# Kernel optimization log

Hardware: AMD Instinct MI355X
Metric: run time of the kernel (lower is better)

## Reference

```python
import jax, jax.numpy as jnp
import numpy as np

MIN_NORM = 1e-15
BALL_EPS = 4e-3  # fp32 boundary eps used by HGCN PoincareBall.proj
C = 1.0
RATIO = 0.75


def _norm(x):
    return jnp.clip(jnp.sqrt(jnp.sum(x * x, axis=-1, keepdims=True)), MIN_NORM)


def artanh(x):
    return jnp.arctanh(jnp.clip(x, -1.0 + 1e-7, 1.0 - 1e-7))


def proj(x, c):
    n = _norm(x)
    maxnorm = (1.0 - BALL_EPS) / jnp.sqrt(c)
    return jnp.where(n > maxnorm, x / n * maxnorm, x)


def expmap0(u, c):
    sc = jnp.sqrt(c)
    un = _norm(u)
    return jnp.tanh(sc * un) * u / (sc * un)


def logmap0(p, c):
    sc = jnp.sqrt(c)
    pn = _norm(p)
    return artanh(sc * pn) * p / (sc * pn)


def mobius_matvec(m, x, c):
    sc = jnp.sqrt(c)
    xn = _norm(x)
    mx = x @ m.T  # [N, out]
    mxn = _norm(mx)
    res = jnp.tanh(mxn / xn * artanh(sc * xn)) * mx / (mxn * sc)
    zero = jnp.all(mx == 0, axis=-1, keepdims=True)
    return jnp.where(zero, jnp.zeros_like(res), res)


def mobius_add(x, y, c):
    x2 = jnp.sum(x * x, axis=-1, keepdims=True)
    y2 = jnp.sum(y * y, axis=-1, keepdims=True)
    xy = jnp.sum(x * y, axis=-1, keepdims=True)
    num = (1 + 2 * c * xy + c * y2) * x + (1 - c * x2) * y
    den = 1 + 2 * c * xy + c * c * x2 * y2
    return num / jnp.maximum(den, MIN_NORM)


def hyp_linear(x, W, b, c):
    res = proj(mobius_matvec(W, x, c), c)
    hb = proj(expmap0(b[None, :], c), c)  # proj_tan0 is identity in Poincare ball
    return proj(mobius_add(res, hb, c), c)


def setup_inputs() -> dict:
    key = jax.random.key(0)
    k = jax.random.split(key, 6)
    N, E, D_IN, D_OUT = 50000, 800000, 128, 64
    x = 0.01 * jax.random.normal(k[0], (N, D_IN), jnp.float32)  # points near origin of ball
    W = jax.random.normal(k[1], (D_OUT, D_IN), jnp.float32) * np.sqrt(2.0 / (D_IN + D_OUT))
    b = 0.01 * jax.random.normal(k[2], (D_OUT,), jnp.float32)
    beta_W = jax.random.normal(k[3], (1, 2 * D_OUT), jnp.float32) * np.sqrt(2.0 / (2 * D_OUT + 1))
    beta_b = 0.01 * jax.random.normal(k[4], (1,), jnp.float32)
    edge_index = jax.random.randint(k[5], (2, E), 0, N, dtype=jnp.int64)
    return {"x": x, "W": W, "b": b, "beta_W": beta_W, "beta_b": beta_b, "edge_index": edge_index}


def reference(x, W, b, beta_W, beta_b, edge_index):
    N = x.shape[0]
    src, dst = edge_index[0], edge_index[1]  # PyG: x_j = x[src], aggregated at dst
    agg = lambda v: jax.ops.segment_sum(v[src], dst, num_segments=N)

    updated_x = hyp_linear(x, W, b, C)
    updated_tanx = logmap0(updated_x, C)

    # NodeInformationScore: (I - D^{-1/2} A D^{-1/2}) x, self loops removed (weight 0)
    w = jnp.where(src == dst, 0.0, 1.0).astype(x.dtype)
    deg = jax.ops.segment_sum(w, src, num_segments=N)
    dinv = jnp.where(deg > 0, deg ** -0.5, 0.0)
    norm_e = dinv[src] * w * dinv[dst]  # [E]
    neigh = jax.ops.segment_sum(norm_e[:, None] * updated_tanx[src], dst, num_segments=N)
    info = updated_tanx - neigh
    score = jnp.sum(jnp.abs(info), axis=1)  # [N]

    k = int(N * RATIO)
    T = jax.lax.top_k(score, k)[0][-1]  # min of top-k values
    sel = (score > T).astype(x.dtype)[:, None]  # [N, 1] hard gate

    sum_neigh = agg(updated_tanx)
    sum_sel = agg(sel * updated_tanx)
    concat = jnp.concatenate([sum_sel, sum_neigh], axis=-1)  # [N, 2*out]
    hyp_sums = proj(expmap0(concat, C), C)

    beta_out = hyp_linear(hyp_sums, beta_W, beta_b, C)  # [N, 1]
    w_sel = jax.nn.sigmoid(logmap0(beta_out, C))  # [N, 1]

    A_x = jax.nn.relu(agg(w_sel * sel * updated_tanx))
    out = proj(expmap0(updated_tanx + A_x, C), C)
    return out
```

## Files before the change

kernel.cpp:

```cpp
#include <hip/hip_runtime.h>
#include <math.h>
#include <limits.h>


__device__ __forceinline__ float wredsum(float v) {
#pragma unroll
    for (int off = 32; off > 0; off >>= 1) v += __shfl_xor(v, off, 64);
    return v;
}

__device__ __forceinline__ float rdlane_f(float v, int i) {
    return __uint_as_float(__builtin_amdgcn_readlane(__float_as_uint(v), i));
}

__device__ __forceinline__ int bitonic64(int val, int lane) {
#pragma unroll
    for (int k = 2; k <= 64; k <<= 1) {
#pragma unroll
        for (int j = k >> 1; j > 0; j >>= 1) {
            int other = __shfl_xor(val, j, 64);
            bool asc = ((lane & k) == 0);
            bool lower = ((lane & j) == 0);
            val = (asc == lower) ? min(val, other) : max(val, other);
        }
    }
    return val;
}

__device__ __forceinline__ float artanh_pos(float z) {
    z = fminf(z, 1.0f - 1e-7f);
    return 0.5f * (log1pf(z) - log1pf(-z));
}

__device__ __forceinline__ unsigned short f2bf(float f) {
    unsigned u = __float_as_uint(f);
    unsigned r = 0x7FFFu + ((u >> 16) & 1u);
    return (unsigned short)((u + r) >> 16);
}
__device__ __forceinline__ float bf2f(unsigned short h) {
    return __uint_as_float(((unsigned)h) << 16);
}

#define MAXNORM 0.996f
#define MINNORM 1e-15f
#define SLOT    64
#define GRP_CAP 5120


__global__ void k_transW(const float* __restrict__ W, float* __restrict__ WT) {
    int idx = blockIdx.x * 256 + threadIdx.x;
    if (idx >= 64 * 128) return;
    int o = idx >> 7, k = idx & 127;
    WT[k * 64 + o] = W[idx];
}


__global__ __launch_bounds__(256) void k_linear(
    const float* __restrict__ x, const float* __restrict__ WTg,
    const float* __restrict__ b, float* __restrict__ utx,
    unsigned short* __restrict__ utx16, int N)
{
    __shared__ float wt[8192];
    __shared__ float xq4[4][64];
    __shared__ float hb_s[64];
    int tid = threadIdx.x;
    int wave = tid >> 6, lane = tid & 63;
    int wave_u = __builtin_amdgcn_readfirstlane(wave);
    int r_hi = lane >> 3, o_hi = lane & 7;

    {
        const float4* src = (const float4*)WTg;
        float4* dst = (float4*)wt;
        for (int i = tid; i < 2048; i += 256) dst[i] = src[i];
    }
    if (wave == 0) {
        float bv = b[lane];
        float bn = fmaxf(sqrtf(wredsum(bv * bv)), MINNORM);
        float h = tanhf(bn) / bn * bv;
        float hn = fmaxf(sqrtf(wredsum(h * h)), MINNORM);
        if (hn > MAXNORM) h *= MAXNORM / hn;
        hb_s[lane] = h;
    }
    __syncthreads();

    int rbase = blockIdx.x * 64;
    const float4* xr4[8];
#pragma unroll
    for (int j = 0; j < 8; ++j)
        xr4[j] = (const float4*)(x + (size_t)min(rbase + r_hi * 8 + j, N - 1) * 128);

    float acc[64];
#pragma unroll
    for (int e = 0; e < 64; ++e) acc[e] = 0.f;
    float xsq8[8];
#pragma unroll
    for (int j = 0; j < 8; ++j) xsq8[j] = 0.f;

    int kb = wave_u * 32;
    for (int q = 0; q < 8; ++q) {
        int c = wave_u * 8 + q;
        float4 xq[8];
#pragma unroll
        for (int j = 0; j < 8; ++j)
            xq[j] = xr4[j][c];
        float wreg[4][8];
#pragma unroll
        for (int i = 0; i < 4; ++i) {
            float4 lo = *(const float4*)(wt + (kb + q * 4 + i) * 64 + o_hi * 8);
            float4 hi = *(const float4*)(wt + (kb + q * 4 + i) * 64 + o_hi * 8 + 4);
            wreg[i][0] = lo.x; wreg[i][1] = lo.y; wreg[i][2] = lo.z; wreg[i][3] = lo.w;
            wreg[i][4] = hi.x; wreg[i][5] = hi.y; wreg[i][6] = hi.z; wreg[i][7] = hi.w;
        }
#pragma unroll
        for (int j = 0; j < 8; ++j) {
#pragma unroll
            for (int oj = 0; oj < 8; ++oj) {
                acc[j * 8 + oj] += xq[j].x * wreg[0][oj] + xq[j].y * wreg[1][oj]
                                 + xq[j].z * wreg[2][oj] + xq[j].w * wreg[3][oj];
            }
            xsq8[j] += xq[j].x * xq[j].x + xq[j].y * xq[j].y
                     + xq[j].z * xq[j].z + xq[j].w * xq[j].w;
        }
    }

    if (o_hi == 0) {
#pragma unroll
        for (int j = 0; j < 8; ++j) xq4[wave_u][r_hi * 8 + j] = xsq8[j];
    }
    __syncthreads();

    float* redp = wt;
#pragma unroll
    for (int c = 0; c < 4; ++c) {
        if (wave_u != 0) {
#pragma unroll
            for (int r = 0; r < 16; ++r) redp[(wave_u - 1) * 1024 + r * 64 + lane] = acc[c * 16 + r];
        }
        __syncthreads();
        if (wave_u == 0) {
#pragma unroll
            for (int r = 0; r < 16; ++r)
                acc[c * 16 + r] += redp[0 * 1024 + r * 64 + lane]
                                 + redp[1 * 1024 + r * 64 + lane]
                                 + redp[2 * 1024 + r * 64 + lane];
        }
        __syncthreads();
    }

    float* eT = wt + 3072;
    if (wave_u == 0) {
#pragma unroll
        for (int j = 0; j < 8; ++j) {
            float4 v0 = { acc[j * 8 + 0], acc[j * 8 + 1], acc[j * 8 + 2], acc[j * 8 + 3] };
            float4 v1 = { acc[j * 8 + 4], acc[j * 8 + 5], acc[j * 8 + 6], acc[j * 8 + 7] };
            *(float4*)(eT + (r_hi * 8 + j) * 68 + o_hi * 8) = v0;
            *(float4*)(eT + (r_hi * 8 + j) * 68 + o_hi * 8 + 4) = v1;
        }
    }
    __syncthreads();
    if (wave_u != 0) return;

    float a2[64];
#pragma unroll
    for (int c4 = 0; c4 < 16; ++c4) {
        float4 v = *(const float4*)(eT + lane * 68 + c4 * 4);
        a2[c4 * 4 + 0] = v.x; a2[c4 * 4 + 1] = v.y;
        a2[c4 * 4 + 2] = v.z; a2[c4 * 4 + 3] = v.w;
    }
    float xsq = xq4[0][lane];
    xsq += xq4[1][lane] + xq4[2][lane] + xq4[3][lane];

    int row = blockIdx.x * 64 + lane;
    bool valid = row < N;

    float mx2 = 0.f;
#pragma unroll
    for (int o = 0; o < 64; ++o) mx2 += a2[o] * a2[o];

    float xn  = fmaxf(sqrtf(xsq), MINNORM);
    float mxn = fmaxf(sqrtf(mx2), MINNORM);
    float fac = tanhf(mxn / xn * artanh_pos(xn)) / mxn;
    float rn  = fac * mxn;
    if (rn > MAXNORM) { fac *= MAXNORM / rn; rn = MAXNORM; }
    float x2 = rn * rn;

    float hv_ = hb_s[lane];
    float hb2 = wredsum(hv_ * hv_);

    float xy = 0.f;
#pragma unroll
    for (int o = 0; o < 64; ++o) xy += (fac * a2[o]) * hb_s[o];

    float den = fmaxf(1.f + 2.f * xy + x2 * hb2, MINNORM);
    float ca  = (1.f + 2.f * xy + hb2) / den;
    float cb  = (1.f - x2) / den;

    float pn2 = 0.f;
#pragma unroll
    for (int o = 0; o < 64; ++o) {
        float p = ca * (fac * a2[o]) + cb * hb_s[o];
        a2[o] = p;
        pn2 += p * p;
    }
    float pn  = fmaxf(sqrtf(pn2), MINNORM);
    float psc = (pn > MAXNORM) ? (MAXNORM / pn) : 1.0f;
    float qn  = fmaxf(pn * psc, MINNORM);
    float lfac = artanh_pos(qn) / qn * psc;

    if (valid) {
        float* orow = utx + (size_t)row * 64;
        unsigned short* orow16 = utx16 + (size_t)row * 64;
#pragma unroll
        for (int o = 0; o < 64; o += 4) {
            float4 ov = { a2[o] * lfac, a2[o + 1] * lfac,
                          a2[o + 2] * lfac, a2[o + 3] * lfac };
            *(float4*)(orow + o) = ov;
            ushort4 hv = { f2bf(ov.x), f2bf(ov.y), f2bf(ov.z), f2bf(ov.w) };
            *(ushort4*)(orow16 + o) = hv;
        }
    }
}


__global__ __launch_bounds__(256) void k_partA(
    const int* __restrict__ ei, int E,
    int* cursD, int* cursS, unsigned* __restrict__ recD,
    unsigned char* __restrict__ recS)
{
    __shared__ int hD[256], hS[256], bD[256], bS[256];
    int tid = threadIdx.x;
    hD[tid] = 0; hS[tid] = 0;
    __syncthreads();
    int base = blockIdx.x * 4096;
    int sv[16], dv[16];
#pragma unroll
    for (int i = 0; i < 16; ++i) {
        int e = base + tid + i * 256;
        if (e < E) {
            sv[i] = ei[e]; dv[i] = ei[E + e];
            atomicAdd(&hD[dv[i] >> 8], 1);
            if (sv[i] != dv[i]) atomicAdd(&hS[sv[i] >> 8], 1);
        } else sv[i] = -1;
    }
    __syncthreads();
    if (hD[tid]) bD[tid] = atomicAdd(&cursD[tid], hD[tid]);
    if (hS[tid]) bS[tid] = atomicAdd(&cursS[tid], hS[tid]);
    __syncthreads();
    hD[tid] = 0; hS[tid] = 0;
    __syncthreads();
#pragma unroll
    for (int i = 0; i < 16; ++i) {
        if (sv[i] < 0) continue;
        int gD = dv[i] >> 8;
        int p = bD[gD] + atomicAdd(&hD[gD], 1);
        if (p < GRP_CAP)
            recD[(size_t)gD * GRP_CAP + p] = (unsigned)sv[i] | ((unsigned)(dv[i] & 255) << 16);
        if (sv[i] != dv[i]) {
            int gS = sv[i] >> 8;
            int q = bS[gS] + atomicAdd(&hS[gS], 1);
            if (q < GRP_CAP)
                recS[(size_t)gS * GRP_CAP + q] = (unsigned char)(sv[i] & 255);
        }
    }
}

__global__ __launch_bounds__(256) void k_Bdeg(
    const int* __restrict__ cursS, const unsigned char* __restrict__ recS,
    float* __restrict__ dinv, int N)
{
    __shared__ unsigned h[256];
    int g = blockIdx.x, tid = threadIdx.x;
    h[tid] = 0;
    __syncthreads();
    int m = min(cursS[g], GRP_CAP);
    const unsigned char* r = recS + (size_t)g * GRP_CAP;
    for (int i = tid; i < m; i += 256) atomicAdd(&h[r[i]], 1u);
    __syncthreads();
    int n = g * 256 + tid;
    if (n < N) {
        unsigned dg = h[tid];
        dinv[n] = dg > 0 ? 1.0f / sqrtf((float)dg) : 0.0f;
    }
}

__global__ __launch_bounds__(256) void k_Bscat(
    const int* __restrict__ cursD, const unsigned* __restrict__ recD,
    int* __restrict__ cnt, int* __restrict__ slots, int N)
{
    __shared__ int lcnt[256];
    __shared__ int lslot[256 * SLOT];
    int g = blockIdx.x, tid = threadIdx.x;
    lcnt[tid] = 0;
    __syncthreads();
    int m = min(cursD[g], GRP_CAP);
    const unsigned* r = recD + (size_t)g * GRP_CAP;
    for (int i = tid; i < m; i += 256) {
        unsigned v = r[i];
        int dlo = v >> 16, s = (int)(v & 0xFFFFu);
        int p = atomicAdd(&lcnt[dlo], 1);
        if (p < SLOT) lslot[dlo * SLOT + p] = s;
    }
    __syncthreads();
    int nbase = g * 256;
    if (nbase + tid < N) cnt[nbase + tid] = lcnt[tid];
    int wave = tid >> 6, lane = tid & 63;
    for (int j = 0; j < 64; ++j) {
        int node = wave * 64 + j;
        if (nbase + node >= N) break;
        int d = min(lcnt[node], SLOT);
        if (lane < d)
            slots[(size_t)(nbase + node) * SLOT + lane] = lslot[node * SLOT + lane];
    }
}


__global__ __launch_bounds__(256) void k_pass1(
    const float* __restrict__ utx, const int* __restrict__ cnt,
    const int* __restrict__ slots, const float* __restrict__ dinv,
    float* __restrict__ score, float* __restrict__ sumn, int N)
{
    int wid = (blockIdx.x * 256 + threadIdx.x) >> 6;
    int lane = threadIdx.x & 63;
    if (wid >= N) return;
    int d = min(cnt[wid], SLOT);
    int val = (lane < d) ? slots[(size_t)wid * SLOT + lane] : INT_MAX;
    val = bitonic64(val, lane);
    int sval = (lane < d) ? val : wid;
    float dn = dinv[wid];
    float wv = (lane < d && sval != wid) ? dn * dinv[sval] : 0.f;
    float wn = (lane < d) ? 1.0f : 0.0f;

    float accn = 0.f, accs = 0.f;
    for (int i0 = 0; i0 < d; i0 += 8) {
#pragma unroll
        for (int j = 0; j < 8; ++j) {
            int i = i0 + j;
            int   s = __builtin_amdgcn_readlane(sval, i);
            float w = rdlane_f(wv, i);
            float n = rdlane_f(wn, i);
            float v = utx[(size_t)s * 64 + lane];
            accn += w * v;
            accs += n * v;
        }
    }
    float info = utx[(size_t)wid * 64 + lane] - accn;
    float sc = wredsum(fabsf(info));
    sumn[(size_t)wid * 64 + lane] = accs;
    if (lane == 0) score[wid] = sc;
}


__global__ __launch_bounds__(256) void k_hist8(
    const float* __restrict__ score, unsigned* __restrict__ hist,
    const unsigned* __restrict__ scal, int N, int pass)
{
    __shared__ unsigned lh[256];
    int tid = threadIdx.x;
    lh[tid] = 0;
    __syncthreads();
    int n = blockIdx.x * 256 + tid;
    if (n < N) {
        unsigned bits = __float_as_uint(score[n]);
        bool active = (pass == 0) || (((bits ^ scal[0]) >> (32 - 8 * pass)) == 0u);
        if (active) atomicAdd(&lh[(bits >> (24 - 8 * pass)) & 0xFFu], 1u);
    }
    __syncthreads();
    unsigned c = lh[tid];
    if (c) atomicAdd(&hist[tid], c);
}

__global__ __launch_bounds__(256) void k_pick8(
    const unsigned* __restrict__ hist, unsigned* scal, int K, int pass)
{
    __shared__ unsigned h[256];
    int t = threadIdx.x;
    h[t] = hist[t];
    __syncthreads();
    if (t == 0) {
        unsigned R = (pass == 0) ? (unsigned)K : scal[1];
        unsigned acc = 0;
        int B = 0;
        for (int bin = 255; bin >= 0; --bin) {
            if (acc + h[bin] >= R) { B = bin; break; }
            acc += h[bin];
        }
        unsigned prefix = (pass == 0) ? 0u : scal[0];
        scal[0] = prefix | ((unsigned)B << (24 - 8 * pass));
        scal[1] = R - acc;
        if (pass == 3) scal[2] = scal[0];
    }
}


__global__ __launch_bounds__(256) void k_sums_corr(
    const unsigned short* __restrict__ utx16, const int* __restrict__ cnt,
    const int* __restrict__ slots, const float* __restrict__ score,
    const unsigned* __restrict__ scal,
    const float* __restrict__ sumn, float* __restrict__ sums, int N)
{
    int wid = (blockIdx.x * 256 + threadIdx.x) >> 6;
    int lane = threadIdx.x & 63;
    if (wid >= N) return;
    float T = __uint_as_float(scal[2]);
    int d = min(cnt[wid], SLOT);
    int val = (lane < d) ? slots[(size_t)wid * SLOT + lane] : INT_MAX;
    val = bitonic64(val, lane);
    int sval = (lane < d) ? val : wid;
    float wc = (lane < d) ? ((score[sval] > T) ? 0.0f : 1.0f) : 0.0f;

    float corr = 0.f;
    for (int i0 = 0; i0 < d; i0 += 8) {
#pragma unroll
        for (int j = 0; j < 8; ++j) {
            int i = i0 + j;
            float w = rdlane_f(wc, i);
            int   s = __builtin_amdgcn_readlane(sval, i);
            if (w != 0.f)
                corr += bf2f(utx16[(size_t)s * 64 + lane]);
        }
    }
    size_t o = (size_t)wid * 64 + lane;
    sums[o] = sumn[o] - corr;
}


__global__ __launch_bounds__(256) void k_beta(
    const float* __restrict__ sumn, const float* __restrict__ sums,
    const float* __restrict__ beta_W, const float* __restrict__ beta_b,
    const float* __restrict__ score, const unsigned* __restrict__ scal,
    float* __restrict__ wsel, int N)
{
    int n = blockIdx.x * 256 + threadIdx.x;
    if (n >= N) return;
    const float4* su4 = (const float4*)(sums + (size_t)n * 64);
    const float4* sn4 = (const float4*)(sumn + (size_t)n * 64);
    float s_uu = 0.f, s_ub = 0.f;
#pragma unroll
    for (int k4 = 0; k4 < 16; ++k4) {
        float4 u0 = su4[k4];
        float4 u1 = sn4[k4];
        float4 b0 = *(const float4*)(beta_W + k4 * 4);
        float4 b1 = *(const float4*)(beta_W + 64 + k4 * 4);
        s_uu += u0.x * u0.x + u0.y * u0.y + u0.z * u0.z + u0.w * u0.w
              + u1.x * u1.x + u1.y * u1.y + u1.z * u1.z + u1.w * u1.w;
        s_ub += u0.x * b0.x + u0.y * b0.y + u0.z * b0.z + u0.w * b0.w
              + u1.x * b1.x + u1.y * b1.y + u1.z * b1.z + u1.w * b1.w;
    }
    float un = fmaxf(sqrtf(s_uu), MINNORM);
    float f  = tanhf(un) / un;
    float hn = fmaxf(f * un, MINNORM);
    float psc1 = (hn > MAXNORM) ? (MAXNORM / hn) : 1.0f;
    float xn = fmaxf(hn * psc1, MINNORM);
    float mx = f * psc1 * s_ub;
    float mxn = fmaxf(fabsf(mx), MINNORM);
    float res = tanhf(mxn / xn * artanh_pos(xn)) * mx / mxn;
    float rn = fmaxf(fabsf(res), MINNORM);
    if (rn > MAXNORM) res = res / rn * MAXNORM;
    float bb = beta_b[0];
    float bn = fmaxf(fabsf(bb), MINNORM);
    float hb = tanhf(bn) / bn * bb;
    float hbn = fmaxf(fabsf(hb), MINNORM);
    if (hbn > MAXNORM) hb = hb / hbn * MAXNORM;
    float x2 = res * res, y2 = hb * hb, xy = res * hb;
    float num = (1.f + 2.f * xy + y2) * res + (1.f - x2) * hb;
    float den = 1.f + 2.f * xy + x2 * y2;
    float p = num / fmaxf(den, MINNORM);
    float pn = fmaxf(fabsf(p), MINNORM);
    if (pn > MAXNORM) p = p / pn * MAXNORM;
    float qn = fmaxf(fabsf(p), MINNORM);
    float lg = artanh_pos(qn) * p / qn;
    float w = 1.f / (1.f + expf(-lg));
    float T = __uint_as_float(scal[2]);
    wsel[n] = (score[n] > T) ? w : 0.0f;
}


__global__ __launch_bounds__(256) void k_axout(
    const float* __restrict__ utx, const unsigned short* __restrict__ utx16,
    const int* __restrict__ cnt, const int* __restrict__ slots,
    const float* __restrict__ wsel, float* __restrict__ out, int N)
{
    int wid = (blockIdx.x * 256 + threadIdx.x) >> 6;
    int lane = threadIdx.x & 63;
    if (wid >= N) return;
    int d = min(cnt[wid], SLOT);
    int val = (lane < d) ? slots[(size_t)wid * SLOT + lane] : INT_MAX;
    val = bitonic64(val, lane);
    int sval = (lane < d) ? val : wid;
    float wa = (lane < d) ? wsel[sval] : 0.0f;

    float acc = 0.f;
    for (int i0 = 0; i0 < d; i0 += 8) {
#pragma unroll
        for (int j = 0; j < 8; ++j) {
            int i = i0 + j;
            int   s = __builtin_amdgcn_readlane(sval, i);
            float w = rdlane_f(wa, i);
            acc += w * bf2f(utx16[(size_t)s * 64 + lane]);
        }
    }
    float a = fmaxf(acc, 0.f);
    float u = utx[(size_t)wid * 64 + lane] + a;
    float un = fmaxf(sqrtf(wredsum(u * u)), MINNORM);
    float o = tanhf(un) / un * u;
    float on = fmaxf(sqrtf(wredsum(o * o)), MINNORM);
    if (on > MAXNORM) o *= MAXNORM / on;
    out[(size_t)wid * 64 + lane] = o;
}


extern "C" void kernel_launch(void* const* d_in, const int* in_sizes, int n_in,
                              void* d_out, int out_size, void* d_ws, size_t ws_size,
                              hipStream_t stream)
{
    const float* x      = (const float*)d_in[0];
    const float* W      = (const float*)d_in[1];
    const float* b      = (const float*)d_in[2];
    const float* beta_W = (const float*)d_in[3];
    const float* beta_b = (const float*)d_in[4];
    const int*   ei     = (const int*)d_in[5];

    const int N = in_sizes[0] / 128;
    const int E = in_sizes[5] / 2;
    const int K = (int)((double)N * 0.75);
    float* out = (float*)d_out;

    char* ws = (char*)d_ws;
    size_t off = 0;
    auto alloc = [&](size_t bytes) -> void* {
        void* p = ws + off;
        off = (off + bytes + 255) & ~(size_t)255;
        return p;
    };
    float*          utx    = (float*)alloc((size_t)N * 64 * 4);
    unsigned short* utx16  = (unsigned short*)alloc((size_t)N * 64 * 2);
    float*          sumn   = (float*)alloc((size_t)N * 64 * 4);
    float*          sums   = (float*)alloc((size_t)N * 64 * 4);
    float*          score  = (float*)alloc((size_t)N * 4);
    float*          dinv   = (float*)alloc((size_t)N * 4);
    float*          wsel   = (float*)alloc((size_t)N * 4);
    int*            cnt    = (int*)alloc((size_t)N * 4);
    int*            slots  = (int*)alloc((size_t)N * SLOT * 4);
    float*          WT     = (float*)alloc(64 * 128 * 4);
    unsigned*       hist8  = (unsigned*)alloc(4 * 256 * 4);
    unsigned*       scal   = (unsigned*)alloc(64);
    int*            cursD  = (int*)alloc(256 * 4);
    int*            cursS  = (int*)alloc(256 * 4);
    if (off > ws_size) return;

    const int gG = (N + 255) / 256;
    unsigned*       recD = (unsigned*)sums;
    unsigned char*  recS = (unsigned char*)sums + (size_t)gG * GRP_CAP * 4;

    hipMemsetAsync(cursD, 0, 256 * 4, stream);
    hipMemsetAsync(cursS, 0, 256 * 4, stream);
    hipMemsetAsync(hist8, 0, 4 * 256 * 4, stream);

    int gN  = (N + 255) / 256;
    int gW  = (N + 3) / 4;
    int gLin = (N + 63) / 64;
    int gA  = (E + 4095) / 4096;

    k_transW<<<32, 256, 0, stream>>>(W, WT);
    k_linear<<<gLin, 256, 0, stream>>>(x, WT, b, utx, utx16, N);
    k_partA<<<gA, 256, 0, stream>>>(ei, E, cursD, cursS, recD, recS);
    k_Bdeg<<<gG, 256, 0, stream>>>(cursS, recS, dinv, N);
    k_Bscat<<<gG, 256, 0, stream>>>(cursD, recD, cnt, slots, N);
    k_pass1<<<gW, 256, 0, stream>>>(utx, cnt, slots, dinv, score, sumn, N);
    for (int pass = 0; pass < 4; ++pass) {
        k_hist8<<<gN, 256, 0, stream>>>(score, hist8 + 256 * pass, scal, N, pass);
        k_pick8<<<1, 256, 0, stream>>>(hist8 + 256 * pass, scal, K, pass);
    }
    k_sums_corr<<<gW, 256, 0, stream>>>(utx16, cnt, slots, score, scal, sumn, sums, N);
    k_beta<<<gN, 256, 0, stream>>>(sumn, sums, beta_W, beta_b, score, scal, wsel, N);
    k_axout<<<gW, 256, 0, stream>>>(utx, utx16, cnt, slots, wsel, out, N);
}
```

Baseline: 259.6 us.

## Fuse graph build, radix-select pick, and beta gating kernels to cut launches

Merges the degree and scatter kernels into one pass over the bucketed records. Folds the per-pass pick into the histogram kernel using a last-block-done atomic counter. Fuses the correction and beta-gating kernels so the selected sums stay in registers, which removes the N×64 sums buffer write and read. The three memsets become a single contiguous memset, and the record buffers get their own allocation. This saves about seven launches and some global traffic, at the cost of a threadfence and atomic handshake per histogram block and only lane 0 doing the beta math per wave.

Result: slower. 310.1 us (+19.4%).

```diff
diff --git a/kernel.cpp b/kernel.cpp
--- a/kernel.cpp
+++ b/kernel.cpp
@@ -264,34 +264,20 @@
     }
 }
 
-__global__ __launch_bounds__(256) void k_Bdeg(
+__global__ __launch_bounds__(256) void k_Bfused(
+    const int* __restrict__ cursD, const unsigned* __restrict__ recD,
     const int* __restrict__ cursS, const unsigned char* __restrict__ recS,
-    float* __restrict__ dinv, int N)
-{
-    __shared__ unsigned h[256];
-    int g = blockIdx.x, tid = threadIdx.x;
-    h[tid] = 0;
-    __syncthreads();
-    int m = min(cursS[g], GRP_CAP);
-    const unsigned char* r = recS + (size_t)g * GRP_CAP;
-    for (int i = tid; i < m; i += 256) atomicAdd(&h[r[i]], 1u);
-    __syncthreads();
-    int n = g * 256 + tid;
-    if (n < N) {
-        unsigned dg = h[tid];
-        dinv[n] = dg > 0 ? 1.0f / sqrtf((float)dg) : 0.0f;
-    }
-}
-
-__global__ __launch_bounds__(256) void k_Bscat(
-    const int* __restrict__ cursD, const unsigned* __restrict__ recD,
-    int* __restrict__ cnt, int* __restrict__ slots, int N)
+    int* __restrict__ cnt, int* __restrict__ slots, float* __restrict__ dinv, int N)
 {
     __shared__ int lcnt[256];
     __shared__ int lslot[256 * SLOT];
+    __shared__ unsigned hdeg[256];
     int g = blockIdx.x, tid = threadIdx.x;
-    lcnt[tid] = 0;
-    __syncthreads();
+    lcnt[tid] = 0; hdeg[tid] = 0;
+    __syncthreads();
+    int mS = min(cursS[g], GRP_CAP);
+    const unsigned char* rS = recS + (size_t)g * GRP_CAP;
+    for (int i = tid; i < mS; i += 256) atomicAdd(&hdeg[rS[i]], 1u);
     int m = min(cursD[g], GRP_CAP);
     const unsigned* r = recD + (size_t)g * GRP_CAP;
     for (int i = tid; i < m; i += 256) {
@@ -302,7 +288,11 @@
     }
     __syncthreads();
     int nbase = g * 256;
-    if (nbase + tid < N) cnt[nbase + tid] = lcnt[tid];
+    if (nbase + tid < N) {
+        cnt[nbase + tid] = lcnt[tid];
+        unsigned dg = hdeg[tid];
+        dinv[nbase + tid] = dg > 0 ? 1.0f / sqrtf((float)dg) : 0.0f;
+    }
     int wave = tid >> 6, lane = tid & 63;
     for (int j = 0; j < 64; ++j) {
         int node = wave * 64 + j;
@@ -350,11 +340,12 @@
 }
 
 
-__global__ __launch_bounds__(256) void k_hist8(
+__global__ __launch_bounds__(256) void k_histpick(
     const float* __restrict__ score, unsigned* __restrict__ hist,
-    const unsigned* __restrict__ scal, int N, int pass)
+    unsigned* scal, unsigned* done, int N, int K, int pass)
 {
     __shared__ unsigned lh[256];
+    __shared__ int lastblk;
     int tid = threadIdx.x;
     lh[tid] = 0;
     __syncthreads();
@@ -367,22 +358,19 @@
     __syncthreads();
     unsigned c = lh[tid];
     if (c) atomicAdd(&hist[tid], c);
-}
-
-__global__ __launch_bounds__(256) void k_pick8(
-    const unsigned* __restrict__ hist, unsigned* scal, int K, int pass)
-{
-    __shared__ unsigned h[256];
-    int t = threadIdx.x;
-    h[t] = hist[t];
-    __syncthreads();
-    if (t == 0) {
+    __threadfence();
+    if (tid == 0) lastblk = (atomicAdd(done, 1u) == (unsigned)(gridDim.x - 1));
+    __syncthreads();
+    if (!lastblk) return;
+    lh[tid] = atomicAdd(&hist[tid], 0u);
+    __syncthreads();
+    if (tid == 0) {
         unsigned R = (pass == 0) ? (unsigned)K : scal[1];
         unsigned acc = 0;
         int B = 0;
         for (int bin = 255; bin >= 0; --bin) {
-            if (acc + h[bin] >= R) { B = bin; break; }
-            acc += h[bin];
+            if (acc + lh[bin] >= R) { B = bin; break; }
+            acc += lh[bin];
         }
         unsigned prefix = (pass == 0) ? 0u : scal[0];
         scal[0] = prefix | ((unsigned)B << (24 - 8 * pass));
@@ -392,11 +380,12 @@
 }
 
 
-__global__ __launch_bounds__(256) void k_sums_corr(
+__global__ __launch_bounds__(256) void k_corrbeta(
     const unsigned short* __restrict__ utx16, const int* __restrict__ cnt,
     const int* __restrict__ slots, const float* __restrict__ score,
-    const unsigned* __restrict__ scal,
-    const float* __restrict__ sumn, float* __restrict__ sums, int N)
+    const unsigned* __restrict__ scal, const float* __restrict__ sumn,
+    const float* __restrict__ beta_W, const float* __restrict__ beta_b,
+    float* __restrict__ wsel, int N)
 {
     int wid = (blockIdx.x * 256 + threadIdx.x) >> 6;
     int lane = threadIdx.x & 63;
@@ -419,59 +408,39 @@
                 corr += bf2f(utx16[(size_t)s * 64 + lane]);
         }
     }
-    size_t o = (size_t)wid * 64 + lane;
-    sums[o] = sumn[o] - corr;
-}
-
-
-__global__ __launch_bounds__(256) void k_beta(
-    const float* __restrict__ sumn, const float* __restrict__ sums,
-    const float* __restrict__ beta_W, const float* __restrict__ beta_b,
-    const float* __restrict__ score, const unsigned* __restrict__ scal,
-    float* __restrict__ wsel, int N)
-{
-    int n = blockIdx.x * 256 + threadIdx.x;
-    if (n >= N) return;
-    const float4* su4 = (const float4*)(sums + (size_t)n * 64);
-    const float4* sn4 = (const float4*)(sumn + (size_t)n * 64);
-    float s_uu = 0.f, s_ub = 0.f;
-#pragma unroll
-    for (int k4 = 0; k4 < 16; ++k4) {
-        float4 u0 = su4[k4];
-        float4 u1 = sn4[k4];
-        float4 b0 = *(const float4*)(beta_W + k4 * 4);
-        float4 b1 = *(const float4*)(beta_W + 64 + k4 * 4);
-        s_uu += u0.x * u0.x + u0.y * u0.y + u0.z * u0.z + u0.w * u0.w
-              + u1.x * u1.x + u1.y * u1.y + u1.z * u1.z + u1.w * u1.w;
-        s_ub += u0.x * b0.x + u0.y * b0.y + u0.z * b0.z + u0.w * b0.w
-              + u1.x * b1.x + u1.y * b1.y + u1.z * b1.z + u1.w * b1.w;
-    }
-    float un = fmaxf(sqrtf(s_uu), MINNORM);
-    float f  = tanhf(un) / un;
-    float hn = fmaxf(f * un, MINNORM);
-    float psc1 = (hn > MAXNORM) ? (MAXNORM / hn) : 1.0f;
-    float xn = fmaxf(hn * psc1, MINNORM);
-    float mx = f * psc1 * s_ub;
-    float mxn = fmaxf(fabsf(mx), MINNORM);
-    float res = tanhf(mxn / xn * artanh_pos(xn)) * mx / mxn;
-    float rn = fmaxf(fabsf(res), MINNORM);
-    if (rn > MAXNORM) res = res / rn * MAXNORM;
-    float bb = beta_b[0];
-    float bn = fmaxf(fabsf(bb), MINNORM);
-    float hb = tanhf(bn) / bn * bb;
-    float hbn = fmaxf(fabsf(hb), MINNORM);
-    if (hbn > MAXNORM) hb = hb / hbn * MAXNORM;
-    float x2 = res * res, y2 = hb * hb, xy = res * hb;
-    float num = (1.f + 2.f * xy + y2) * res + (1.f - x2) * hb;
-    float den = 1.f + 2.f * xy + x2 * y2;
-    float p = num / fmaxf(den, MINNORM);
-    float pn = fmaxf(fabsf(p), MINNORM);
-    if (pn > MAXNORM) p = p / pn * MAXNORM;
-    float qn = fmaxf(fabsf(p), MINNORM);
-    float lg = artanh_pos(qn) * p / qn;
-    float w = 1.f / (1.f + expf(-lg));
-    float T = __uint_as_float(scal[2]);
-    wsel[n] = (score[n] > T) ? w : 0.0f;
+    float u1 = sumn[(size_t)wid * 64 + lane];
+    float u0 = u1 - corr;
+    float bw0 = beta_W[lane], bw1 = beta_W[64 + lane];
+    float s_uu = wredsum(u0 * u0 + u1 * u1);
+    float s_ub = wredsum(u0 * bw0 + u1 * bw1);
+
+    if (lane == 0) {
+        float un = fmaxf(sqrtf(s_uu), MINNORM);
+        float f  = tanhf(un) / un;
+        float hn = fmaxf(f * un, MINNORM);
+        float psc1 = (hn > MAXNORM) ? (MAXNORM / hn) : 1.0f;
+        float xn = fmaxf(hn * psc1, MINNORM);
+        float mx = f * psc1 * s_ub;
+        float mxn = fmaxf(fabsf(mx), MINNORM);
+        float res = tanhf(mxn / xn * artanh_pos(xn)) * mx / mxn;
+        float rn = fmaxf(fabsf(res), MINNORM);
+        if (rn > MAXNORM) res = res / rn * MAXNORM;
+        float bb = beta_b[0];
+        float bn = fmaxf(fabsf(bb), MINNORM);
+        float hb = tanhf(bn) / bn * bb;
+        float hbn = fmaxf(fabsf(hb), MINNORM);
+        if (hbn > MAXNORM) hb = hb / hbn * MAXNORM;
+        float x2 = res * res, y2 = hb * hb, xy = res * hb;
+        float num = (1.f + 2.f * xy + y2) * res + (1.f - x2) * hb;
+        float den = 1.f + 2.f * xy + x2 * y2;
+        float p = num / fmaxf(den, MINNORM);
+        float pn = fmaxf(fabsf(p), MINNORM);
+        if (pn > MAXNORM) p = p / pn * MAXNORM;
+        float qn = fmaxf(fabsf(p), MINNORM);
+        float lg = artanh_pos(qn) * p / qn;
+        float w = 1.f / (1.f + expf(-lg));
+        wsel[wid] = (score[wid] > T) ? w : 0.0f;
+    }
 }
 
 
@@ -524,6 +493,8 @@
     const int E = in_sizes[5] / 2;
     const int K = (int)((double)N * 0.75);
     float* out = (float*)d_out;
+
+    const int gG = (N + 255) / 256;
 
     char* ws = (char*)d_ws;
     size_t off = 0;
@@ -535,26 +506,24 @@
     float*          utx    = (float*)alloc((size_t)N * 64 * 4);
     unsigned short* utx16  = (unsigned short*)alloc((size_t)N * 64 * 2);
     float*          sumn   = (float*)alloc((size_t)N * 64 * 4);
-    float*          sums   = (float*)alloc((size_t)N * 64 * 4);
     float*          score  = (float*)alloc((size_t)N * 4);
     float*          dinv   = (float*)alloc((size_t)N * 4);
     float*          wsel   = (float*)alloc((size_t)N * 4);
     int*            cnt    = (int*)alloc((size_t)N * 4);
     int*            slots  = (int*)alloc((size_t)N * SLOT * 4);
     float*          WT     = (float*)alloc(64 * 128 * 4);
+    unsigned*       recD   = (unsigned*)alloc((size_t)gG * GRP_CAP * 4);
+    unsigned char*  recS   = (unsigned char*)alloc((size_t)gG * GRP_CAP);
+    unsigned*       scal   = (unsigned*)alloc(64);
+    char*           zbase  = (char*)alloc(0);
     unsigned*       hist8  = (unsigned*)alloc(4 * 256 * 4);
-    unsigned*       scal   = (unsigned*)alloc(64);
+    unsigned*       done4  = (unsigned*)alloc(4 * 4);
     int*            cursD  = (int*)alloc(256 * 4);
     int*            cursS  = (int*)alloc(256 * 4);
+    size_t          zbytes = (size_t)(((char*)(cursS + 256)) - zbase);
     if (off > ws_size) return;
 
-    const int gG = (N + 255) / 256;
-    unsigned*       recD = (unsigned*)sums;
-    unsigned char*  recS = (unsigned char*)sums + (size_t)gG * GRP_CAP * 4;
-
-    hipMemsetAsync(cursD, 0, 256 * 4, stream);
-    hipMemsetAsync(cursS, 0, 256 * 4, stream);
-    hipMemsetAsync(hist8, 0, 4 * 256 * 4, stream);
+    hipMemsetAsync(zbase, 0, zbytes, stream);
 
     int gN  = (N + 255) / 256;
     int gW  = (N + 3) / 4;
@@ -564,14 +533,12 @@
     k_transW<<<32, 256, 0, stream>>>(W, WT);
     k_linear<<<gLin, 256, 0, stream>>>(x, WT, b, utx, utx16, N);
     k_partA<<<gA, 256, 0, stream>>>(ei, E, cursD, cursS, recD, recS);
-    k_Bdeg<<<gG, 256, 0, stream>>>(cursS, recS, dinv, N);
-    k_Bscat<<<gG, 256, 0, stream>>>(cursD, recD, cnt, slots, N);
+    k_Bfused<<<gG, 256, 0, stream>>>(cursD, recD, cursS, recS, cnt, slots, dinv, N);
     k_pass1<<<gW, 256, 0, stream>>>(utx, cnt, slots, dinv, score, sumn, N);
-    for (int pass = 0; pass < 4; ++pass) {
-        k_hist8<<<gN, 256, 0, stream>>>(score, hist8 + 256 * pass, scal, N, pass);
-        k_pick8<<<1, 256, 0, stream>>>(hist8 + 256 * pass, scal, K, pass);
-    }
-    k_sums_corr<<<gW, 256, 0, stream>>>(utx16, cnt, slots, score, scal, sumn, sums, N);
-    k_beta<<<gN, 256, 0, stream>>>(sumn, sums, beta_W, beta_b, score, scal, wsel, N);
+    for (int pass = 0; pass < 4; ++pass)
+        k_histpick<<<gN, 256, 0, stream>>>(score, hist8 + 256 * pass, scal,
+                                           done4 + pass, N, K, pass);
+    k_corrbeta<<<gW, 256, 0, stream>>>(utx16, cnt, slots, score, scal, sumn,
+                                       beta_W, beta_b, wsel, N);
     k_axout<<<gW, 256, 0, stream>>>(utx, utx16, cnt, slots, wsel, out, N);
 }
```
